# Kernel tuning notes

Hardware: AMD Instinct MI355X
Metric: run time of the kernel (lower is better)

Reference implementation:

```python
import jax, jax.numpy as jnp
import numpy as np

NUM_ROUTES, NUM_TIME, DIM, K, C = 100000, 2016, 256, 100, 5
BATCH = 262144


def _xavier(key, shape):
    fan_in, fan_out = shape[0], shape[1]
    lim = np.sqrt(6.0 / (fan_in + fan_out))
    return jax.random.uniform(key, shape, jnp.float32, -lim, lim)


def setup_inputs() -> dict:
    key = jax.random.key(0)
    ks = jax.random.split(key, 9)
    route_idx = jax.random.randint(ks[0], (BATCH,), 0, NUM_ROUTES)
    time_idx = jax.random.randint(ks[1], (BATCH,), 0, NUM_TIME)
    route_table = _xavier(ks[2], (NUM_ROUTES, DIM))
    time_table = _xavier(ks[3], (NUM_TIME, DIM))
    w = _xavier(ks[4], (DIM, K))
    mode_a = _xavier(ks[5], (DIM, C))
    mode_b = _xavier(ks[6], (DIM, C))
    mode_bias = jnp.zeros((C, C), jnp.float32)
    fc_lim = 1.0 / np.sqrt(C * C + K)
    fc_w = jax.random.uniform(ks[7], (C * C + K, 1), jnp.float32, -fc_lim, fc_lim)
    fc_b = jax.random.uniform(ks[8], (1,), jnp.float32, -fc_lim, fc_lim)
    return {
        "route_idx": route_idx, "time_idx": time_idx,
        "route_table": route_table, "time_table": time_table,
        "w": w, "mode_a": mode_a, "mode_b": mode_b,
        "mode_bias": mode_bias, "fc_w": fc_w, "fc_b": fc_b,
    }


def reference(route_idx, time_idx, route_table, time_table, w, mode_a, mode_b, mode_bias, fc_w, fc_b):
    r = route_table[route_idx]            # [B, D]
    t = time_table[time_idx]              # [B, D]
    gcp = jax.nn.relu((r * t) @ w)        # [B, K]
    # einsum('ni,nj->nij') then contracting i with mode_a and j with mode_b
    # equals outer product of the two small projections (exact same math):
    ra = r @ mode_a                       # [B, C]
    tb = t @ mode_b                       # [B, C]
    inter = jax.nn.sigmoid(ra[:, :, None] * tb[:, None, :] + mode_bias)  # [B, C, C]
    feats = jnp.concatenate([gcp, inter.reshape(inter.shape[0], -1)], axis=1)  # [B, K + C*C]
    out = feats @ fc_w + fc_b             # [B, 1]
    return jnp.squeeze(out, axis=-1)      # [B]
```

## Files before the change

kernel.cpp:

```cpp
#include <hip/hip_runtime.h>
#include <stdint.h>

#define BATCH   262144
#define NROUTES 100000
#define NTIME   2016
#define DIM     256
#define KOUT    100
#define NTILES  7

typedef __attribute__((ext_vector_type(2))) float f32x2;
typedef __attribute__((ext_vector_type(4))) float f32x4;

#define WS_WFRAG_BYTES ((size_t)(NTILES * 8 * 64 * 8))
#define WS_RA_OFF   (WS_WFRAG_BYTES)
#define WS_TB_OFF   (WS_RA_OFF + (size_t)NROUTES * 32)
#define WS_RT8_OFF  (WS_TB_OFF + (size_t)NTIME * 32)
#define WS_TT8_OFF  (WS_RT8_OFF + (size_t)NROUTES * 256)
#define WS_NEED     (WS_TT8_OFF + (size_t)NTIME * 256)

template<int CTRL>
static __device__ __forceinline__ float dpp_add(float x) {
  int s = __builtin_amdgcn_update_dpp(0, __builtin_bit_cast(int, x), CTRL, 0xF, 0xF, true);
  return x + __builtin_bit_cast(float, s);
}
static __device__ __forceinline__ float wave_sum63(float x) {
  x = dpp_add<0x111>(x);
  x = dpp_add<0x112>(x);
  x = dpp_add<0x114>(x);
  x = dpp_add<0x118>(x);
  x = dpp_add<0x142>(x);
  x = dpp_add<0x143>(x);
  return x;
}
static __device__ __forceinline__ float sum16_all(float x) {
  x = dpp_add<0x0B1>(x);
  x = dpp_add<0x04E>(x);
  x = dpp_add<0x124>(x);
  x = dpp_add<0x128>(x);
  return x;
}
static __device__ __forceinline__ float sigm(float z) {
  return __builtin_amdgcn_rcpf(1.0f + __expf(-z));
}

__global__ __launch_bounds__(256) void prep_kernel(
    const float* __restrict__ route_table,
    const float* __restrict__ time_table,
    const float* __restrict__ w,
    const float* __restrict__ mode_a,
    const float* __restrict__ mode_b,
    uint8_t* __restrict__ ws, int do8)
{
  const int b   = blockIdx.x;
  const int tid = threadIdx.x;

  if (b < 14) {
    const int u = b * 256 + tid;
    const int lane = u & 63;
    const int frag = u >> 6;
    const int ks = frag / NTILES;
    const int nt = frag % NTILES;
    const int n  = nt * 16 + (lane & 15);
    const int k0 = ks * 32 + (lane >> 4) * 8;
    float v[8];
    #pragma unroll
    for (int j = 0; j < 8; ++j)
      v[j] = (n < KOUT) ? w[(size_t)(k0 + j) * KOUT + n] : 0.0f;
    uint32_t d0 = 0, d1 = 0;
    d0 = __builtin_amdgcn_cvt_pk_fp8_f32(v[0], v[1], d0, false);
    d0 = __builtin_amdgcn_cvt_pk_fp8_f32(v[2], v[3], d0, true);
    d1 = __builtin_amdgcn_cvt_pk_fp8_f32(v[4], v[5], d1, false);
    d1 = __builtin_amdgcn_cvt_pk_fp8_f32(v[6], v[7], d1, true);
    ((uint2*)ws)[u] = make_uint2(d0, d1);
    return;
  }

  const float* tab; const float* proj; float* outp; uint8_t* out8; int base;
  if (b < 14 + 126) {
    tab = time_table;  proj = mode_b; outp = (float*)(ws + WS_TB_OFF);
    out8 = ws + WS_TT8_OFF; base = (b - 14) * 16;
  } else {
    tab = route_table; proj = mode_a; outp = (float*)(ws + WS_RA_OFF);
    out8 = ws + WS_RT8_OFF; base = (b - 140) * 16;
  }

  const int wave = tid >> 6, lane = tid & 63;
  float A[4][5];
  #pragma unroll
  for (int j = 0; j < 4; ++j)
    #pragma unroll
    for (int i = 0; i < 5; ++i)
      A[j][i] = proj[(4 * lane + j) * 5 + i];

  const int p0 = (lane >> 4) * 64 + ((lane >> 1) & 3) * 16 +
                 ((lane >> 3) & 1) * 8 + (lane & 1) * 4;

  const int row0 = base + wave * 4;
  float4 v[4];
  #pragma unroll
  for (int rr = 0; rr < 4; ++rr)
    v[rr] = *(const float4*)(tab + (size_t)(row0 + rr) * DIM + 4 * lane);

  #pragma unroll
  for (int rr = 0; rr < 4; ++rr) {
    const int row = row0 + rr;
    if (do8) {
      uint32_t u = 0;
      u = __builtin_amdgcn_cvt_pk_fp8_f32(8.f * v[rr].x, 8.f * v[rr].y, u, false);
      u = __builtin_amdgcn_cvt_pk_fp8_f32(8.f * v[rr].z, 8.f * v[rr].w, u, true);
      *(uint32_t*)(out8 + (size_t)row * 256 + p0) = u;
    }
    float p[5];
    #pragma unroll
    for (int i = 0; i < 5; ++i) {
      float s = v[rr].x * A[0][i] + v[rr].y * A[1][i] + v[rr].z * A[2][i] + v[rr].w * A[3][i];
      p[i] = wave_sum63(s);
    }
    if (lane == 63) {
      float* o = outp + (size_t)row * 8;
      *(f32x4*)o = (f32x4){p[0], p[1], p[2], p[3]};
      o[4] = p[4];
    }
  }
}

__global__ __launch_bounds__(256, 2) void main_pipelined(
    const int*   __restrict__ route_idx,
    const int*   __restrict__ time_idx,
    const float* __restrict__ mode_bias,
    const float* __restrict__ fc_w,
    const float* __restrict__ fc_b,
    const uint8_t* __restrict__ ws,
    float* __restrict__ out)
{
  __shared__ uint4 wlds[1792];
  const int tid  = threadIdx.x;
  const int wave = tid >> 6, lane = tid & 63;
  const int col  = lane & 15, quad = lane >> 4;
  const int base = (blockIdx.x * 4 + wave) * 64;

  {
    const uint4* wsrc = (const uint4*)ws;
    #pragma unroll
    for (int j = 0; j < 7; ++j)
      wlds[j * 256 + tid] = wsrc[j * 256 + tid];
  }

  float fcw_l[NTILES];
  #pragma unroll
  for (int nt = 0; nt < NTILES; ++nt) {
    const int n = nt * 16 + col;
    fcw_l[nt] = (n < KOUT) ? fc_w[n] * 0.015625f : 0.0f;
  }
  const float fb = fc_b[0];

  uint4 rw[2][4], tw[2][4];
  f32x4 ra0[2], tb0[2];
  float ra4[2], tb4[2];

  auto issue = [&](int buf, int ri, int ti) {
    const uint8_t* rb = ws + WS_RT8_OFF + (size_t)ri * 256 + quad * 16;
    const uint8_t* tb = ws + WS_TT8_OFF + (size_t)ti * 256 + quad * 16;
    #pragma unroll
    for (int i = 0; i < 4; ++i) {
      rw[buf][i] = *(const uint4*)(rb + i * 64);
      tw[buf][i] = *(const uint4*)(tb + i * 64);
    }
    const float* rap = (const float*)(ws + WS_RA_OFF) + (size_t)ri * 8;
    const float* tbp = (const float*)(ws + WS_TB_OFF) + (size_t)ti * 8;
    ra0[buf] = *(const f32x4*)rap; ra4[buf] = rap[4];
    tb0[buf] = *(const f32x4*)tbp; tb4[buf] = tbp[4];
  };

  int ri_n = route_idx[base + col];
  int ti_n = time_idx[base + col];
  issue(0, ri_n, ti_n);
  ri_n = route_idx[base + 16 + col];
  ti_n = time_idx[base + 16 + col];

  __syncthreads();

  const uint2* wl2 = (const uint2*)wlds;

  #pragma unroll
  for (int it = 0; it < 4; ++it) {
    const int cb = it & 1, nb = cb ^ 1;
    if (it < 3) {
      issue(nb, ri_n, ti_n);
      if (it < 2) {
        ri_n = route_idx[base + (it + 2) * 16 + col];
        ti_n = time_idx[base + (it + 2) * 16 + col];
      }
    }

    f32x4 acc[NTILES];
    #pragma unroll
    for (int nt = 0; nt < NTILES; ++nt) acc[nt] = (f32x4){0.f, 0.f, 0.f, 0.f};

    #pragma unroll
    for (int ks = 0; ks < 8; ++ks) {
      const int i = ks >> 1;
      const uint32_t ra = (ks & 1) ? rw[cb][i].z : rw[cb][i].x;
      const uint32_t rb = (ks & 1) ? rw[cb][i].w : rw[cb][i].y;
      const uint32_t ta = (ks & 1) ? tw[cb][i].z : tw[cb][i].x;
      const uint32_t tb = (ks & 1) ? tw[cb][i].w : tw[cb][i].y;
      f32x2 r01 = __builtin_amdgcn_cvt_pk_f32_fp8(ra, false);
      f32x2 r23 = __builtin_amdgcn_cvt_pk_f32_fp8(ra, true);
      f32x2 r45 = __builtin_amdgcn_cvt_pk_f32_fp8(rb, false);
      f32x2 r67 = __builtin_amdgcn_cvt_pk_f32_fp8(rb, true);
      f32x2 t01 = __builtin_amdgcn_cvt_pk_f32_fp8(ta, false);
      f32x2 t23 = __builtin_amdgcn_cvt_pk_f32_fp8(ta, true);
      f32x2 t45 = __builtin_amdgcn_cvt_pk_f32_fp8(tb, false);
      f32x2 t67 = __builtin_amdgcn_cvt_pk_f32_fp8(tb, true);
      f32x2 x01 = r01 * t01, x23 = r23 * t23, x45 = r45 * t45, x67 = r67 * t67;
      uint32_t p0 = 0, p1 = 0;
      p0 = __builtin_amdgcn_cvt_pk_fp8_f32(x01.x, x01.y, p0, false);
      p0 = __builtin_amdgcn_cvt_pk_fp8_f32(x23.x, x23.y, p0, true);
      p1 = __builtin_amdgcn_cvt_pk_fp8_f32(x45.x, x45.y, p1, false);
      p1 = __builtin_amdgcn_cvt_pk_fp8_f32(x67.x, x67.y, p1, true);
      const long a64 = __builtin_bit_cast(long, make_uint2(p0, p1));
      #pragma unroll
      for (int nt = 0; nt < NTILES; ++nt) {
        const long b64 = __builtin_bit_cast(long, wl2[(ks * NTILES + nt) * 64 + lane]);
        acc[nt] = __builtin_amdgcn_mfma_f32_16x16x32_fp8_fp8(a64, b64, acc[nt], 0, 0, 0);
      }
    }

    float s[4];
    #pragma unroll
    for (int reg = 0; reg < 4; ++reg) {
      float v = 0.f;
      #pragma unroll
      for (int nt = 0; nt < NTILES; ++nt)
        v += fmaxf(acc[nt][reg], 0.f) * fcw_l[nt];
      s[reg] = sum16_all(v);
    }

    const float rav[5] = {ra0[cb].x, ra0[cb].y, ra0[cb].z, ra0[cb].w, ra4[cb]};
    const float tbv[5] = {tb0[cb].x, tb0[cb].y, tb0[cb].z, tb0[cb].w, tb4[cb]};
    const float rq = (quad & 2) ? ((quad & 1) ? rav[3] : rav[2])
                                : ((quad & 1) ? rav[1] : rav[0]);
    const float tq = (quad & 2) ? ((quad & 1) ? tbv[3] : tbv[2])
                                : ((quad & 1) ? tbv[1] : tbv[0]);
    float sig = 0.f;
    #pragma unroll
    for (int j = 0; j < 5; ++j)
      sig += sigm(rq * tbv[j] + mode_bias[5 * quad + j]) * fc_w[KOUT + 5 * quad + j];
    sig += sigm(rav[4] * tq + mode_bias[20 + quad]) * fc_w[KOUT + 20 + quad];
    if (quad == 0)
      sig += sigm(rav[4] * tbv[4] + mode_bias[24]) * fc_w[KOUT + 24];
    sig += __shfl_xor(sig, 16, 64);
    sig += __shfl_xor(sig, 32, 64);

    if (quad == (col >> 2)) {
      const float sa = (col & 1) ? s[1] : s[0];
      const float sb = (col & 1) ? s[3] : s[2];
      const float gcp = (col & 2) ? sb : sa;
      out[base + it * 16 + col] = fb + gcp + sig;
    }
  }
}

__global__ __launch_bounds__(256, 4) void main_fallback(
    const int*   __restrict__ route_idx,
    const int*   __restrict__ time_idx,
    const float* __restrict__ route_table,
    const float* __restrict__ time_table,
    const float* __restrict__ mode_bias,
    const float* __restrict__ fc_w,
    const float* __restrict__ fc_b,
    const uint8_t* __restrict__ ws,
    float* __restrict__ out)
{
  __shared__ uint4 wlds[1792];
  const int tid  = threadIdx.x;
  const int wave = tid >> 6, lane = tid & 63;
  const int col  = lane & 15, quad = lane >> 4;
  const int m0   = blockIdx.x * 64 + wave * 16;
  const size_t ri = (size_t)route_idx[m0 + col];
  const size_t ti = (size_t)time_idx[m0 + col];

  const float* rap = (const float*)(ws + WS_RA_OFF) + ri * 8;
  const float* tbp = (const float*)(ws + WS_TB_OFF) + ti * 8;
  f32x4 ra0 = *(const f32x4*)rap; float ra4 = rap[4];
  f32x4 tb0 = *(const f32x4*)tbp; float tb4 = tbp[4];

  {
    const uint4* wsrc = (const uint4*)ws;
    #pragma unroll
    for (int j = 0; j < 7; ++j)
      wlds[j * 256 + tid] = wsrc[j * 256 + tid];
  }
  __syncthreads();

  float fcw_l[NTILES];
  #pragma unroll
  for (int nt = 0; nt < NTILES; ++nt) {
    const int n = nt * 16 + col;
    fcw_l[nt] = (n < KOUT) ? fc_w[n] * 0.015625f : 0.0f;
  }

  f32x4 acc[NTILES];
  #pragma unroll
  for (int nt = 0; nt < NTILES; ++nt) acc[nt] = (f32x4){0.f, 0.f, 0.f, 0.f};
  const uint2* wl2 = (const uint2*)wlds;

  #pragma unroll
  for (int ks = 0; ks < 8; ++ks) {
    const float4* rp = (const float4*)(route_table + ri * DIM + ks * 32 + quad * 8);
    const float4* tp = (const float4*)(time_table  + ti * DIM + ks * 32 + quad * 8);
    float4 r0 = rp[0], r1 = rp[1], t0 = tp[0], t1 = tp[1];
    uint32_t p0 = 0, p1 = 0;
    p0 = __builtin_amdgcn_cvt_pk_fp8_f32(64.f * r0.x * t0.x, 64.f * r0.y * t0.y, p0, false);
    p0 = __builtin_amdgcn_cvt_pk_fp8_f32(64.f * r0.z * t0.z, 64.f * r0.w * t0.w, p0, true);
    p1 = __builtin_amdgcn_cvt_pk_fp8_f32(64.f * r1.x * t1.x, 64.f * r1.y * t1.y, p1, false);
    p1 = __builtin_amdgcn_cvt_pk_fp8_f32(64.f * r1.z * t1.z, 64.f * r1.w * t1.w, p1, true);
    const long a64 = __builtin_bit_cast(long, make_uint2(p0, p1));
    #pragma unroll
    for (int nt = 0; nt < NTILES; ++nt) {
      const long b64 = __builtin_bit_cast(long, wl2[(ks * NTILES + nt) * 64 + lane]);
      acc[nt] = __builtin_amdgcn_mfma_f32_16x16x32_fp8_fp8(a64, b64, acc[nt], 0, 0, 0);
    }
  }

  float s[4];
  #pragma unroll
  for (int reg = 0; reg < 4; ++reg) {
    float v = 0.f;
    #pragma unroll
    for (int nt = 0; nt < NTILES; ++nt)
      v += fmaxf(acc[nt][reg], 0.f) * fcw_l[nt];
    s[reg] = sum16_all(v);
  }

  const float rav[5] = {ra0.x, ra0.y, ra0.z, ra0.w, ra4};
  const float tbv[5] = {tb0.x, tb0.y, tb0.z, tb0.w, tb4};
  const float rq = (quad & 2) ? ((quad & 1) ? rav[3] : rav[2])
                              : ((quad & 1) ? rav[1] : rav[0]);
  const float tq = (quad & 2) ? ((quad & 1) ? tbv[3] : tbv[2])
                              : ((quad & 1) ? tbv[1] : tbv[0]);
  float sig = 0.f;
  #pragma unroll
  for (int j = 0; j < 5; ++j)
    sig += sigm(rq * tbv[j] + mode_bias[5 * quad + j]) * fc_w[KOUT + 5 * quad + j];
  sig += sigm(rav[4] * tq + mode_bias[20 + quad]) * fc_w[KOUT + 20 + quad];
  if (quad == 0)
    sig += sigm(rav[4] * tbv[4] + mode_bias[24]) * fc_w[KOUT + 24];
  sig += __shfl_xor(sig, 16, 64);
  sig += __shfl_xor(sig, 32, 64);

  if (quad == (col >> 2)) {
    const float sa = (col & 1) ? s[1] : s[0];
    const float sb = (col & 1) ? s[3] : s[2];
    const float gcp = (col & 2) ? sb : sa;
    out[m0 + col] = fc_b[0] + gcp + sig;
  }
}

extern "C" void kernel_launch(void* const* d_in, const int* in_sizes, int n_in,
                              void* d_out, int out_size, void* d_ws, size_t ws_size,
                              hipStream_t stream)
{
  const int*   route_idx   = (const int*)d_in[0];
  const int*   time_idx    = (const int*)d_in[1];
  const float* route_table = (const float*)d_in[2];
  const float* time_table  = (const float*)d_in[3];
  const float* w           = (const float*)d_in[4];
  const float* mode_a      = (const float*)d_in[5];
  const float* mode_b      = (const float*)d_in[6];
  const float* mode_bias   = (const float*)d_in[7];
  const float* fc_w        = (const float*)d_in[8];
  const float* fc_b        = (const float*)d_in[9];
  uint8_t* ws  = (uint8_t*)d_ws;
  float*   out = (float*)d_out;

  const int big = (ws_size >= WS_NEED) ? 1 : 0;

  prep_kernel<<<6390, 256, 0, stream>>>(route_table, time_table, w,
                                        mode_a, mode_b, ws, big);
  if (big)
    main_pipelined<<<BATCH / 256, 256, 0, stream>>>(route_idx, time_idx,
                                                    mode_bias, fc_w, fc_b, ws, out);
  else
    main_fallback<<<BATCH / 64, 256, 0, stream>>>(route_idx, time_idx,
                                                  route_table, time_table,
                                                  mode_bias, fc_w, fc_b, ws, out);
}
```

Before: 203.0 us.

## Double rows per prep block, coalesce fp8 stores, raise main occupancy, prefetch indices

```diff
diff --git a/kernel.cpp b/kernel.cpp
--- a/kernel.cpp
+++ b/kernel.cpp
@@ -43,13 +43,14 @@
   return __builtin_amdgcn_rcpf(1.0f + __expf(-z));
 }
 
+template<int DO8>
 __global__ __launch_bounds__(256) void prep_kernel(
     const float* __restrict__ route_table,
     const float* __restrict__ time_table,
     const float* __restrict__ w,
     const float* __restrict__ mode_a,
     const float* __restrict__ mode_b,
-    uint8_t* __restrict__ ws, int do8)
+    uint8_t* __restrict__ ws)
 {
   const int b   = blockIdx.x;
   const int tid = threadIdx.x;
@@ -76,39 +77,39 @@
   }
 
   const float* tab; const float* proj; float* outp; uint8_t* out8; int base;
-  if (b < 14 + 126) {
+  if (b < 14 + 63) {
     tab = time_table;  proj = mode_b; outp = (float*)(ws + WS_TB_OFF);
-    out8 = ws + WS_TT8_OFF; base = (b - 14) * 16;
+    out8 = ws + WS_TT8_OFF; base = (b - 14) * 32;
   } else {
     tab = route_table; proj = mode_a; outp = (float*)(ws + WS_RA_OFF);
-    out8 = ws + WS_RT8_OFF; base = (b - 140) * 16;
+    out8 = ws + WS_RT8_OFF; base = (b - 77) * 32;
   }
 
   const int wave = tid >> 6, lane = tid & 63;
+  const int perm = (2 * (lane >> 4) + ((lane >> 1) & 1)) * 8 +
+                   ((lane >> 2) & 3) * 2 + (lane & 1);
+
   float A[4][5];
   #pragma unroll
   for (int j = 0; j < 4; ++j)
     #pragma unroll
     for (int i = 0; i < 5; ++i)
-      A[j][i] = proj[(4 * lane + j) * 5 + i];
-
-  const int p0 = (lane >> 4) * 64 + ((lane >> 1) & 3) * 16 +
-                 ((lane >> 3) & 1) * 8 + (lane & 1) * 4;
-
-  const int row0 = base + wave * 4;
-  float4 v[4];
-  #pragma unroll
-  for (int rr = 0; rr < 4; ++rr)
-    v[rr] = *(const float4*)(tab + (size_t)(row0 + rr) * DIM + 4 * lane);
-
-  #pragma unroll
-  for (int rr = 0; rr < 4; ++rr) {
+      A[j][i] = proj[(4 * perm + j) * 5 + i];
+
+  const int row0 = base + wave * 8;
+  float4 v[8];
+  #pragma unroll
+  for (int rr = 0; rr < 8; ++rr)
+    v[rr] = *(const float4*)(tab + (size_t)(row0 + rr) * DIM + 4 * perm);
+
+  #pragma unroll
+  for (int rr = 0; rr < 8; ++rr) {
     const int row = row0 + rr;
-    if (do8) {
+    if (DO8) {
       uint32_t u = 0;
       u = __builtin_amdgcn_cvt_pk_fp8_f32(8.f * v[rr].x, 8.f * v[rr].y, u, false);
       u = __builtin_amdgcn_cvt_pk_fp8_f32(8.f * v[rr].z, 8.f * v[rr].w, u, true);
-      *(uint32_t*)(out8 + (size_t)row * 256 + p0) = u;
+      *(uint32_t*)(out8 + (size_t)row * 256 + 4 * lane) = u;
     }
     float p[5];
     #pragma unroll
@@ -124,7 +125,7 @@
   }
 }
 
-__global__ __launch_bounds__(256, 2) void main_pipelined(
+__global__ __launch_bounds__(256, 3) void main_pipelined(
     const int*   __restrict__ route_idx,
     const int*   __restrict__ time_idx,
     const float* __restrict__ mode_bias,
@@ -139,6 +140,13 @@
   const int col  = lane & 15, quad = lane >> 4;
   const int base = (blockIdx.x * 4 + wave) * 64;
 
+  int ri[4], ti[4];
+  #pragma unroll
+  for (int t = 0; t < 4; ++t) {
+    ri[t] = route_idx[base + t * 16 + col];
+    ti[t] = time_idx[base + t * 16 + col];
+  }
+
   {
     const uint4* wsrc = (const uint4*)ws;
     #pragma unroll
@@ -155,29 +163,17 @@
   const float fb = fc_b[0];
 
   uint4 rw[2][4], tw[2][4];
-  f32x4 ra0[2], tb0[2];
-  float ra4[2], tb4[2];
-
-  auto issue = [&](int buf, int ri, int ti) {
-    const uint8_t* rb = ws + WS_RT8_OFF + (size_t)ri * 256 + quad * 16;
-    const uint8_t* tb = ws + WS_TT8_OFF + (size_t)ti * 256 + quad * 16;
+  auto issue = [&](int buf, int t) {
+    const uint8_t* rb = ws + WS_RT8_OFF + (size_t)ri[t] * 256 + quad * 16;
+    const uint8_t* tb = ws + WS_TT8_OFF + (size_t)ti[t] * 256 + quad * 16;
     #pragma unroll
     for (int i = 0; i < 4; ++i) {
       rw[buf][i] = *(const uint4*)(rb + i * 64);
       tw[buf][i] = *(const uint4*)(tb + i * 64);
     }
-    const float* rap = (const float*)(ws + WS_RA_OFF) + (size_t)ri * 8;
-    const float* tbp = (const float*)(ws + WS_TB_OFF) + (size_t)ti * 8;
-    ra0[buf] = *(const f32x4*)rap; ra4[buf] = rap[4];
-    tb0[buf] = *(const f32x4*)tbp; tb4[buf] = tbp[4];
   };
 
-  int ri_n = route_idx[base + col];
-  int ti_n = time_idx[base + col];
-  issue(0, ri_n, ti_n);
-  ri_n = route_idx[base + 16 + col];
-  ti_n = time_idx[base + 16 + col];
-
+  issue(0, 0);
   __syncthreads();
 
   const uint2* wl2 = (const uint2*)wlds;
@@ -185,13 +181,12 @@
   #pragma unroll
   for (int it = 0; it < 4; ++it) {
     const int cb = it & 1, nb = cb ^ 1;
-    if (it < 3) {
-      issue(nb, ri_n, ti_n);
-      if (it < 2) {
-        ri_n = route_idx[base + (it + 2) * 16 + col];
-        ti_n = time_idx[base + (it + 2) * 16 + col];
-      }
-    }
+
+    const float* rap = (const float*)(ws + WS_RA_OFF) + (size_t)ri[it] * 8;
+    const float* tbp = (const float*)(ws + WS_TB_OFF) + (size_t)ti[it] * 8;
+    f32x4 ra0 = *(const f32x4*)rap; float ra4 = rap[4];
+    f32x4 tb0 = *(const f32x4*)tbp; float tb4 = tbp[4];
+    if (it < 3) issue(nb, it + 1);
 
     f32x4 acc[NTILES];
     #pragma unroll
@@ -236,8 +231,8 @@
       s[reg] = sum16_all(v);
     }
 
-    const float rav[5] = {ra0[cb].x, ra0[cb].y, ra0[cb].z, ra0[cb].w, ra4[cb]};
-    const float tbv[5] = {tb0[cb].x, tb0[cb].y, tb0[cb].z, tb0[cb].w, tb4[cb]};
+    const float rav[5] = {ra0.x, ra0.y, ra0.z, ra0.w, ra4};
+    const float tbv[5] = {tb0.x, tb0.y, tb0.z, tb0.w, tb4};
     const float rq = (quad & 2) ? ((quad & 1) ? rav[3] : rav[2])
                                 : ((quad & 1) ? rav[1] : rav[0]);
     const float tq = (quad & 2) ? ((quad & 1) ? tbv[3] : tbv[2])
@@ -376,13 +371,16 @@
 
   const int big = (ws_size >= WS_NEED) ? 1 : 0;
 
-  prep_kernel<<<6390, 256, 0, stream>>>(route_table, time_table, w,
-                                        mode_a, mode_b, ws, big);
-  if (big)
+  if (big) {
+    prep_kernel<1><<<3202, 256, 0, stream>>>(route_table, time_table, w,
+                                             mode_a, mode_b, ws);
     main_pipelined<<<BATCH / 256, 256, 0, stream>>>(route_idx, time_idx,
                                                     mode_bias, fc_w, fc_b, ws, out);
-  else
+  } else {
+    prep_kernel<0><<<3202, 256, 0, stream>>>(route_table, time_table, w,
+                                             mode_a, mode_b, ws);
     main_fallback<<<BATCH / 64, 256, 0, stream>>>(route_idx, time_idx,
                                                   route_table, time_table,
                                                   mode_bias, fc_w, fc_b, ws, out);
-}
+  }
+}
```

Measured after the change: 201.9 us. Within noise of the previous version (-0.5%).
